# Kernel optimization log

Hardware: AMD Instinct MI355X
Metric: run time of the kernel (lower is better)

Reference implementation:

```python
import jax, jax.numpy as jnp
import numpy as np

H = 512   # LSTM hidden
D = 256   # attention / key dim
V = 33    # output vocab

def _lstm_step(xcat, h, c, W, U, b):
    # Keras LSTMCell: gates ordered i, f, g(candidate), o
    z = xcat @ W + h @ U + b            # [B, 4H]
    i, f, g, o = jnp.split(z, 4, axis=-1)
    i = jax.nn.sigmoid(i); f = jax.nn.sigmoid(f); o = jax.nn.sigmoid(o)
    c_new = f * c + i * jnp.tanh(g)
    h_new = o * jnp.tanh(c_new)
    return h_new, c_new

def _attn(h, keys, Wq, bq):
    # Luong dot attention: query = Dense(h); scores = keys . query; read = softmax . keys
    q = h @ Wq + bq                                # [B, D]
    scores = jnp.einsum('bkd,bd->bk', keys, q)     # [B, K]
    w = jax.nn.softmax(scores, axis=-1)
    return jnp.einsum('bk,bkd->bd', w, keys)       # [B, D]

def setup_inputs() -> dict:
    key = jax.random.key(0)
    ks = jax.random.split(key, 16)
    B, T, K = 256, 256, 512
    s = 0.02
    inp = {
        'x': jax.random.normal(ks[0], (B, T, V), jnp.float32),
        'keys': jax.random.normal(ks[1], (B, K, D), jnp.float32),
        # LSTM 1: input = concat(x[V], attn[D]) -> V+D
        'W1': jax.random.normal(ks[2], (V + D, 4 * H), jnp.float32) * s,
        'U1': jax.random.normal(ks[3], (H, 4 * H), jnp.float32) * s,
        'b1': jnp.zeros((4 * H,), jnp.float32),
        # LSTM 2: input = concat(h1[H], attn1[D]) -> H+D
        'W2': jax.random.normal(ks[4], (H + D, 4 * H), jnp.float32) * s,
        'U2': jax.random.normal(ks[5], (H, 4 * H), jnp.float32) * s,
        'b2': jnp.zeros((4 * H,), jnp.float32),
        # LSTM 3
        'W3': jax.random.normal(ks[6], (H + D, 4 * H), jnp.float32) * s,
        'U3': jax.random.normal(ks[7], (H, 4 * H), jnp.float32) * s,
        'b3': jnp.zeros((4 * H,), jnp.float32),
        # attention query Dense(256) on h[H]
        'Wq': jax.random.normal(ks[8], (H, D), jnp.float32) * s,
        'bq': jnp.zeros((D,), jnp.float32),
        # output Dense(33) on concat(h3[H], attn3[D])
        'Wo': jax.random.normal(ks[9], (H + D, V), jnp.float32) * s,
        'bo': jnp.zeros((V,), jnp.float32),
    }
    return inp

def reference(x, keys, W1, U1, b1, W2, U2, b2, W3, U3, b3, Wq, bq, Wo, bo):
    B, T, _ = x.shape

    def step(carry, x_t):
        h1, c1, h2, c2, h3, c3, a = carry
        inp = jnp.concatenate([x_t, a], axis=-1)          # [B, V+D]
        h1, c1 = _lstm_step(inp, h1, c1, W1, U1, b1)
        a1 = _attn(h1, keys, Wq, bq)
        h2, c2 = _lstm_step(jnp.concatenate([h1, a1], axis=-1), h2, c2, W2, U2, b2)
        a2 = _attn(h2, keys, Wq, bq)
        h3, c3 = _lstm_step(jnp.concatenate([h2, a2], axis=-1), h3, c3, W3, U3, b3)
        a3 = _attn(h3, keys, Wq, bq)
        out = jnp.concatenate([h3, a3], axis=-1) @ Wo + bo  # [B, V]
        return (h1, c1, h2, c2, h3, c3, a3), out

    z = jnp.zeros((B, H), x.dtype)
    carry0 = (z, z, z, z, z, z, jnp.zeros((B, D), x.dtype))
    _, outs = jax.lax.scan(step, carry0, jnp.swapaxes(x, 0, 1))  # outs: [T, B, V]
    return jnp.swapaxes(outs, 0, 1)  # [B, T, V]
```

## Files before the change

kernel.cpp:

```cpp
#include <hip/hip_runtime.h>
#include <hip/hip_bf16.h>
#include <math.h>

#define BB 256
#define TT 256
#define VV 33
#define HH 512
#define DD 256
#define KKEY 512
#define G4 2048
#define K1 832
#define K1A 768
#define K1X 64
#define K2 1280
#define CH 32
#define KP 260

typedef unsigned short u16;
typedef unsigned int u32;
typedef __attribute__((ext_vector_type(8))) short short8;
typedef __attribute__((ext_vector_type(4))) float float4v;

__device__ inline float bf2f(u16 v) {
    union { u32 u; float f; } c; c.u = ((u32)v) << 16; return c.f;
}
__device__ inline u16 f2bf(float f) {
    __hip_bfloat16 h = __float2bfloat16(f);
    union { __hip_bfloat16 h; u16 u; } c; c.h = h; return c.u;
}
__device__ inline void split_bf(float v, u16& hi, u16& lo) {
    hi = f2bf(v);
    lo = f2bf(v - bf2f(hi));
}

__global__ void prep_v7(const float* __restrict__ W, const float* __restrict__ U,
                        u16* __restrict__ WtH, u16* __restrict__ WtL, int Kd, int mode) {
    long idx = (long)blockIdx.x * blockDim.x + threadIdx.x;
    if (idx >= (long)G4 * Kd) return;
    int colp = (int)(idx / Kd);
    int k = (int)(idx % Kd);
    int col = (colp & 3) * 512 + (colp >> 2);
    float v = 0.f;
    if (mode == 1) {
        if (k < 256)      v = W[(long)(33 + k) * G4 + col];
        else if (k < 768) v = U[(long)(k - 256) * G4 + col];
        else if (k < 801) v = W[(long)(k - 768) * G4 + col];
    } else {
        if (k < 768) v = W[(long)k * G4 + col];
        else         v = U[(long)(k - 768) * G4 + col];
    }
    u16 hi, lo; split_bf(v, hi, lo);
    WtH[idx] = hi; WtL[idx] = lo;
}

__global__ void packx_v7(const float* __restrict__ x, u16* __restrict__ xPH, u16* __restrict__ xPL) {
    long idx = (long)blockIdx.x * blockDim.x + threadIdx.x;
    if (idx >= (long)TT * BB * K1X) return;
    int k = (int)(idx % K1X);
    long tb = idx / K1X;
    int b = (int)(tb % BB);
    int t = (int)(tb / BB);
    float v = (k < VV) ? x[((long)b * TT + t) * VV + k] : 0.f;
    u16 hi, lo; split_bf(v, hi, lo);
    xPH[idx] = hi; xPL[idx] = lo;
}

__global__ __launch_bounds__(256, 2) void zg_v8(
    const u16* __restrict__ aH, const u16* __restrict__ aL, int strideA, int Kd,
    const u16* __restrict__ xH, const u16* __restrict__ xL,
    const u16* __restrict__ wH, const u16* __restrict__ wL,
    const float* __restrict__ bias,
    float* __restrict__ c, float* __restrict__ h,
    u16* __restrict__ d0H, u16* __restrict__ d0L, int d0off, int d0stride,
    u16* __restrict__ d1H, u16* __restrict__ d1L, int d1off, int d1stride)
{
    __shared__ u16 AldsH[32 * 40];
    __shared__ u16 AldsL[32 * 40];
    __shared__ u16 WldsH[32 * 40];
    __shared__ u16 WldsL[32 * 40];
    __shared__ float zlds[32 * 36];

    int tid = threadIdx.x;
    int mt = blockIdx.x >> 6;
    int nt = blockIdx.x & 63;
    int M0 = mt * 32, N0 = nt * 32;

    int wave = tid >> 6, lane = tid & 63;
    int lr = lane & 15, lg = lane >> 4;
    int rbase = (wave & 1) * 16, cbase = (wave >> 1) * 16;

    int half = tid >> 7;
    int slot = tid & 127;
    int sr = slot >> 2, sp = slot & 3;

    const u16* aRow = (half ? aL : aH) + (long)(M0 + sr) * strideA;
    const u16* xRow = xH ? ((half ? xL : xH) + (long)(M0 + sr) * K1X) : nullptr;
    const u16* wRow = (half ? wL : wH) + (long)(N0 + sr) * Kd;
    u16* aDst = (half ? AldsL : AldsH) + sr * 40 + sp * 8;
    u16* wDst = (half ? WldsL : WldsH) + sr * 40 + sp * 8;

    float4v acc = (float4v){0.f, 0.f, 0.f, 0.f};

    for (int k0 = 0; k0 < Kd; k0 += 32) {
        int kg = k0 + sp * 8;
        uint4 va = (xRow && kg >= K1A) ? *(const uint4*)(xRow + (kg - K1A))
                                       : *(const uint4*)(aRow + kg);
        uint4 vw = *(const uint4*)(wRow + kg);
        __syncthreads();
        *(uint4*)aDst = va;
        *(uint4*)wDst = vw;
        __syncthreads();
        short8 ah = *(const short8*)(&AldsH[(rbase + lr) * 40 + lg * 8]);
        short8 al = *(const short8*)(&AldsL[(rbase + lr) * 40 + lg * 8]);
        short8 bh = *(const short8*)(&WldsH[(cbase + lr) * 40 + lg * 8]);
        short8 bl = *(const short8*)(&WldsL[(cbase + lr) * 40 + lg * 8]);
        acc = __builtin_amdgcn_mfma_f32_16x16x32_bf16(ah, bh, acc, 0, 0, 0);
        acc = __builtin_amdgcn_mfma_f32_16x16x32_bf16(ah, bl, acc, 0, 0, 0);
        acc = __builtin_amdgcn_mfma_f32_16x16x32_bf16(al, bh, acc, 0, 0, 0);
    }

    #pragma unroll
    for (int r = 0; r < 4; r++)
        zlds[(rbase + lg * 4 + r) * 36 + cbase + lr] = acc[r];
    __syncthreads();

    int um = tid & 7, ml = tid >> 3;
    int u = (nt << 3) + um;
    int m = M0 + ml;
    float zi  = zlds[ml * 36 + um * 4 + 0] + bias[u];
    float zf  = zlds[ml * 36 + um * 4 + 1] + bias[512 + u];
    float zg_ = zlds[ml * 36 + um * 4 + 2] + bias[1024 + u];
    float zo  = zlds[ml * 36 + um * 4 + 3] + bias[1536 + u];
    float i_ = 1.f / (1.f + expf(-zi));
    float f_ = 1.f / (1.f + expf(-zf));
    float g_ = tanhf(zg_);
    float o_ = 1.f / (1.f + expf(-zo));
    long idx = (long)m * HH + u;
    float cn = f_ * c[idx] + i_ * g_;
    c[idx] = cn;
    float hn = o_ * tanhf(cn);
    h[idx] = hn;
    u16 hi_, lo_; split_bf(hn, hi_, lo_);
    if (d0H) {
        d0H[(long)m * d0stride + d0off + u] = hi_;
        d0L[(long)m * d0stride + d0off + u] = lo_;
    }
    d1H[(long)m * d1stride + d1off + u] = hi_;
    d1L[(long)m * d1stride + d1off + u] = lo_;
}

__global__ __launch_bounds__(256) void qattn_v8(
    const float* __restrict__ h, const float* __restrict__ Wq,
    const float* __restrict__ bq, const float* __restrict__ keys,
    u16* __restrict__ dH, u16* __restrict__ dL, int doff, int dstride,
    const float* __restrict__ Wo, const float* __restrict__ bo,
    float* __restrict__ out, int t)
{
    __shared__ __align__(16) float hlds[HH];
    __shared__ __align__(16) float qlds[DD];
    __shared__ __align__(16) float klds[CH * KP];
    __shared__ __align__(16) float slds[CH];
    __shared__ __align__(16) float plds[CH];
    __shared__ __align__(16) float alds[DD];

    int b = blockIdx.x, tid = threadIdx.x;
    int lane = tid & 63, wave = tid >> 6;

    hlds[tid]       = h[(long)b * HH + tid];
    hlds[tid + 256] = h[(long)b * HH + 256 + tid];
    __syncthreads();

    {
        float s0 = 0.f, s1 = 0.f, s2 = 0.f, s3 = 0.f;
        #pragma unroll 8
        for (int j = 0; j < HH; j += 4) {
            s0 += hlds[j]     * Wq[(long)j * DD + tid];
            s1 += hlds[j + 1] * Wq[(long)(j + 1) * DD + tid];
            s2 += hlds[j + 2] * Wq[(long)(j + 2) * DD + tid];
            s3 += hlds[j + 3] * Wq[(long)(j + 3) * DD + tid];
        }
        qlds[tid] = (s0 + s1) + (s2 + s3) + bq[tid];
    }
    __syncthreads();

    const float* kb = keys + (long)b * KKEY * DD;
    float4 q4 = *(const float4*)(&qlds[lane * 4]);

    float m_run = -INFINITY, l_run = 0.f, acc = 0.f;

    float4 kv[8];
    #pragma unroll
    for (int i = 0; i < 8; i++)
        kv[i] = *(const float4*)(kb + (long)(wave + 4 * i) * DD + lane * 4);

    for (int k0 = 0; k0 < KKEY; k0 += CH) {
        __syncthreads();
        float pp[8];
        #pragma unroll
        for (int i = 0; i < 8; i++) {
            *(float4*)(&klds[(wave + 4 * i) * KP + lane * 4]) = kv[i];
            pp[i] = kv[i].x * q4.x + kv[i].y * q4.y + kv[i].z * q4.z + kv[i].w * q4.w;
        }
        float4 kn[8];
        if (k0 + CH < KKEY) {
            #pragma unroll
            for (int i = 0; i < 8; i++)
                kn[i] = *(const float4*)(kb + (long)(k0 + CH + wave + 4 * i) * DD + lane * 4);
        }
        #pragma unroll
        for (int i = 0; i < 8; i++) {
            float s = pp[i];
            s += __shfl_xor(s, 32); s += __shfl_xor(s, 16); s += __shfl_xor(s, 8);
            s += __shfl_xor(s, 4);  s += __shfl_xor(s, 2);  s += __shfl_xor(s, 1);
            if (lane == i) slds[wave + 4 * i] = s;
        }
        __syncthreads();
        float mc = slds[0];
        #pragma unroll
        for (int k = 1; k < CH; k++) mc = fmaxf(mc, slds[k]);
        float m_new = fmaxf(m_run, mc);
        float scale = expf(m_run - m_new);
        if (tid < CH) plds[tid] = expf(slds[tid] - m_new);
        __syncthreads();
        float lsum = 0.f, a0 = 0.f, a1 = 0.f;
        #pragma unroll
        for (int k = 0; k < CH; k += 4) {
            float4 p4 = *(const float4*)(&plds[k]);
            lsum += (p4.x + p4.y) + (p4.z + p4.w);
            a0 += p4.x * klds[(k + 0) * KP + tid] + p4.z * klds[(k + 2) * KP + tid];
            a1 += p4.y * klds[(k + 1) * KP + tid] + p4.w * klds[(k + 3) * KP + tid];
        }
        acc = acc * scale + (a0 + a1);
        l_run = l_run * scale + lsum;
        m_run = m_new;
        #pragma unroll
        for (int i = 0; i < 8; i++) kv[i] = kn[i];
    }

    float av = acc / l_run;
    u16 hi_, lo_; split_bf(av, hi_, lo_);
    dH[(long)b * dstride + doff + tid] = hi_;
    dL[(long)b * dstride + doff + tid] = lo_;

    if (Wo) {
        alds[tid] = av;
        __syncthreads();
        for (int v = wave; v < VV; v += 4) {
            float s = 0.f;
            for (int i = lane; i < HH; i += 64) s += hlds[i] * Wo[(long)i * VV + v];
            for (int i = lane; i < DD; i += 64) s += alds[i] * Wo[(long)(HH + i) * VV + v];
            for (int o = 32; o > 0; o >>= 1) s += __shfl_xor(s, o);
            if (lane == 0) out[((long)b * TT + t) * VV + v] = s + bo[v];
        }
    }
}


extern "C" void kernel_launch(void* const* d_in, const int* in_sizes, int n_in,
                              void* d_out, int out_size, void* d_ws, size_t ws_size,
                              hipStream_t stream) {
    const float *x = nullptr, *keys = nullptr, *W1 = nullptr, *U1 = nullptr,
                *b1 = nullptr, *W2 = nullptr, *U2 = nullptr, *b2 = nullptr,
                *W3 = nullptr, *U3 = nullptr, *b3 = nullptr, *Wq = nullptr,
                *bq = nullptr, *Wo = nullptr, *bo = nullptr;
    {
        int cW23 = 0, cU = 0, cb = 0;
        for (int i = 0; i < n_in; i++) {
            const float* q = (const float*)d_in[i];
            switch (in_sizes[i]) {
                case 2162688:  x = q; break;
                case 33554432: keys = q; break;
                case 591872:   W1 = q; break;
                case 1572864:  if (cW23 == 0) W2 = q; else W3 = q; cW23++; break;
                case 1048576:  if (cU == 0) U1 = q; else if (cU == 1) U2 = q; else U3 = q; cU++; break;
                case 2048:     if (cb == 0) b1 = q; else if (cb == 1) b2 = q; else b3 = q; cb++; break;
                case 131072:   Wq = q; break;
                case 256:      bq = q; break;
                case 25344:    Wo = q; break;
                case 33:       bo = q; break;
                default: break;
            }
        }
    }
    float* out = (float*)d_out;

    char* p = (char*)d_ws;
    auto alloc = [&](size_t n) { char* r = p; p += (n + 255) & ~(size_t)255; return r; };
    u16* WtH1 = (u16*)alloc((size_t)G4 * K1 * 2);
    u16* WtL1 = (u16*)alloc((size_t)G4 * K1 * 2);
    u16* WtH2 = (u16*)alloc((size_t)G4 * K2 * 2);
    u16* WtL2 = (u16*)alloc((size_t)G4 * K2 * 2);
    u16* WtH3 = (u16*)alloc((size_t)G4 * K2 * 2);
    u16* WtL3 = (u16*)alloc((size_t)G4 * K2 * 2);
    u16* xPH = (u16*)alloc((size_t)TT * BB * K1X * 2);
    u16* xPL = (u16*)alloc((size_t)TT * BB * K1X * 2);
    u16* xc1H[2]; u16* xc1L[2]; u16* xc2H[2]; u16* xc2L[2]; u16* xc3H[2]; u16* xc3L[2];
    for (int i = 0; i < 2; i++) {
        xc1H[i] = (u16*)alloc((size_t)BB * K1A * 2);
        xc1L[i] = (u16*)alloc((size_t)BB * K1A * 2);
        xc2H[i] = (u16*)alloc((size_t)BB * K2 * 2);
        xc2L[i] = (u16*)alloc((size_t)BB * K2 * 2);
        xc3H[i] = (u16*)alloc((size_t)BB * K2 * 2);
        xc3L[i] = (u16*)alloc((size_t)BB * K2 * 2);
    }
    float* h1 = (float*)alloc((size_t)BB * HH * 4);
    float* c1 = (float*)alloc((size_t)BB * HH * 4);
    float* h2 = (float*)alloc((size_t)BB * HH * 4);
    float* c2 = (float*)alloc((size_t)BB * HH * 4);
    float* h3 = (float*)alloc((size_t)BB * HH * 4);
    float* c3 = (float*)alloc((size_t)BB * HH * 4);

    {
        long t1 = (long)G4 * K1;
        prep_v7<<<(int)((t1 + 255) / 256), 256, 0, stream>>>(W1, U1, WtH1, WtL1, K1, 1);
        long t2 = (long)G4 * K2;
        prep_v7<<<(int)((t2 + 255) / 256), 256, 0, stream>>>(W2, U2, WtH2, WtL2, K2, 2);
        prep_v7<<<(int)((t2 + 255) / 256), 256, 0, stream>>>(W3, U3, WtH3, WtL3, K2, 2);
        long tx = (long)TT * BB * K1X;
        packx_v7<<<(int)((tx + 255) / 256), 256, 0, stream>>>(x, xPH, xPL);
        hipMemsetAsync(c1, 0, (size_t)BB * HH * 4, stream);
        hipMemsetAsync(c2, 0, (size_t)BB * HH * 4, stream);
        hipMemsetAsync(c3, 0, (size_t)BB * HH * 4, stream);
        hipMemsetAsync(xc1H[0], 0, (size_t)BB * K1A * 2, stream);
        hipMemsetAsync(xc1L[0], 0, (size_t)BB * K1A * 2, stream);
        hipMemsetAsync(xc2H[0], 0, (size_t)BB * K2 * 2, stream);
        hipMemsetAsync(xc2L[0], 0, (size_t)BB * K2 * 2, stream);
        hipMemsetAsync(xc3H[0], 0, (size_t)BB * K2 * 2, stream);
        hipMemsetAsync(xc3L[0], 0, (size_t)BB * K2 * 2, stream);
    }

    for (int t = 0; t < TT; t++) {
        int cur = t & 1, nxt = cur ^ 1;
        zg_v8<<<512, 256, 0, stream>>>(
            xc1H[cur], xc1L[cur], K1A, K1,
            xPH + (long)t * BB * K1X, xPL + (long)t * BB * K1X,
            WtH1, WtL1, b1, c1, h1,
            xc2H[cur], xc2L[cur], 0, K2,
            xc1H[nxt], xc1L[nxt], 256, K1A);
        qattn_v8<<<BB, 256, 0, stream>>>(h1, Wq, bq, keys,
            xc2H[cur], xc2L[cur], 512, K2,
            nullptr, nullptr, nullptr, 0);
        zg_v8<<<512, 256, 0, stream>>>(
            xc2H[cur], xc2L[cur], K2, K2, nullptr, nullptr,
            WtH2, WtL2, b2, c2, h2,
            xc3H[cur], xc3L[cur], 0, K2,
            xc2H[nxt], xc2L[nxt], 768, K2);
        qattn_v8<<<BB, 256, 0, stream>>>(h2, Wq, bq, keys,
            xc3H[cur], xc3L[cur], 512, K2,
            nullptr, nullptr, nullptr, 0);
        zg_v8<<<512, 256, 0, stream>>>(
            xc3H[cur], xc3L[cur], K2, K2, nullptr, nullptr,
            WtH3, WtL3, b3, c3, h3,
            nullptr, nullptr, 0, 0,
            xc3H[nxt], xc3L[nxt], 768, K2);
        qattn_v8<<<BB, 256, 0, stream>>>(h3, Wq, bq, keys,
            xc1H[nxt], xc1L[nxt], 0, K1A,
            Wo, bo, out, t);
    }
}
```

Baseline: 61.20 ms.

## Move attention query projection to MFMA GEMM, prefetch zg tiles, drop softmax max

```diff
diff --git a/kernel.cpp b/kernel.cpp
--- a/kernel.cpp
+++ b/kernel.cpp
@@ -53,6 +53,15 @@
     WtH[idx] = hi; WtL[idx] = lo;
 }
 
+__global__ void prep_wq(const float* __restrict__ Wq,
+                        u16* __restrict__ WqTH, u16* __restrict__ WqTL) {
+    int idx = blockIdx.x * blockDim.x + threadIdx.x;
+    if (idx >= DD * HH) return;
+    int d = idx / HH, j = idx % HH;
+    u16 hi, lo; split_bf(Wq[(long)j * DD + d], hi, lo);
+    WqTH[idx] = hi; WqTL[idx] = lo;
+}
+
 __global__ void packx_v7(const float* __restrict__ x, u16* __restrict__ xPH, u16* __restrict__ xPL) {
     long idx = (long)blockIdx.x * blockDim.x + threadIdx.x;
     if (idx >= (long)TT * BB * K1X) return;
@@ -65,7 +74,7 @@
     xPH[idx] = hi; xPL[idx] = lo;
 }
 
-__global__ __launch_bounds__(256, 2) void zg_v8(
+__global__ __launch_bounds__(256, 2) void zg_v9(
     const u16* __restrict__ aH, const u16* __restrict__ aL, int strideA, int Kd,
     const u16* __restrict__ xH, const u16* __restrict__ xL,
     const u16* __restrict__ wH, const u16* __restrict__ wL,
@@ -99,16 +108,25 @@
     u16* aDst = (half ? AldsL : AldsH) + sr * 40 + sp * 8;
     u16* wDst = (half ? WldsL : WldsH) + sr * 40 + sp * 8;
 
+    auto loadA = [&](int kg) -> uint4 {
+        return (xRow && kg >= K1A) ? *(const uint4*)(xRow + (kg - K1A))
+                                   : *(const uint4*)(aRow + kg);
+    };
+
     float4v acc = (float4v){0.f, 0.f, 0.f, 0.f};
 
+    uint4 va = loadA(sp * 8);
+    uint4 vw = *(const uint4*)(wRow + sp * 8);
+
     for (int k0 = 0; k0 < Kd; k0 += 32) {
-        int kg = k0 + sp * 8;
-        uint4 va = (xRow && kg >= K1A) ? *(const uint4*)(xRow + (kg - K1A))
-                                       : *(const uint4*)(aRow + kg);
-        uint4 vw = *(const uint4*)(wRow + kg);
         __syncthreads();
         *(uint4*)aDst = va;
         *(uint4*)wDst = vw;
+        if (k0 + 32 < Kd) {
+            int kg = k0 + 32 + sp * 8;
+            va = loadA(kg);
+            vw = *(const uint4*)(wRow + kg);
+        }
         __syncthreads();
         short8 ah = *(const short8*)(&AldsH[(rbase + lr) * 40 + lg * 8]);
         short8 al = *(const short8*)(&AldsL[(rbase + lr) * 40 + lg * 8]);
@@ -149,44 +167,85 @@
     d1L[(long)m * d1stride + d1off + u] = lo_;
 }
 
-__global__ __launch_bounds__(256) void qattn_v8(
-    const float* __restrict__ h, const float* __restrict__ Wq,
-    const float* __restrict__ bq, const float* __restrict__ keys,
+__global__ __launch_bounds__(256) void qg_v9(
+    const u16* __restrict__ aH, const u16* __restrict__ aL, int strideA,
+    const u16* __restrict__ wH, const u16* __restrict__ wL,
+    const float* __restrict__ bq, float* __restrict__ qout)
+{
+    __shared__ u16 AldsH[32 * 40];
+    __shared__ u16 AldsL[32 * 40];
+    __shared__ u16 WldsH[32 * 40];
+    __shared__ u16 WldsL[32 * 40];
+
+    int tid = threadIdx.x;
+    int mt = blockIdx.x >> 3;
+    int nt = blockIdx.x & 7;
+    int M0 = mt * 32, N0 = nt * 32;
+
+    int wave = tid >> 6, lane = tid & 63;
+    int lr = lane & 15, lg = lane >> 4;
+    int rbase = (wave & 1) * 16, cbase = (wave >> 1) * 16;
+
+    int half = tid >> 7;
+    int slot = tid & 127;
+    int sr = slot >> 2, sp = slot & 3;
+
+    const u16* aRow = (half ? aL : aH) + (long)(M0 + sr) * strideA;
+    const u16* wRow = (half ? wL : wH) + (long)(N0 + sr) * HH;
+    u16* aDst = (half ? AldsL : AldsH) + sr * 40 + sp * 8;
+    u16* wDst = (half ? WldsL : WldsH) + sr * 40 + sp * 8;
+
+    float4v acc = (float4v){0.f, 0.f, 0.f, 0.f};
+
+    uint4 va = *(const uint4*)(aRow + sp * 8);
+    uint4 vw = *(const uint4*)(wRow + sp * 8);
+
+    for (int k0 = 0; k0 < HH; k0 += 32) {
+        __syncthreads();
+        *(uint4*)aDst = va;
+        *(uint4*)wDst = vw;
+        if (k0 + 32 < HH) {
+            int kg = k0 + 32 + sp * 8;
+            va = *(const uint4*)(aRow + kg);
+            vw = *(const uint4*)(wRow + kg);
+        }
+        __syncthreads();
+        short8 ah = *(const short8*)(&AldsH[(rbase + lr) * 40 + lg * 8]);
+        short8 al = *(const short8*)(&AldsL[(rbase + lr) * 40 + lg * 8]);
+        short8 bh = *(const short8*)(&WldsH[(cbase + lr) * 40 + lg * 8]);
+        short8 bl = *(const short8*)(&WldsL[(cbase + lr) * 40 + lg * 8]);
+        acc = __builtin_amdgcn_mfma_f32_16x16x32_bf16(ah, bh, acc, 0, 0, 0);
+        acc = __builtin_amdgcn_mfma_f32_16x16x32_bf16(ah, bl, acc, 0, 0, 0);
+        acc = __builtin_amdgcn_mfma_f32_16x16x32_bf16(al, bh, acc, 0, 0, 0);
+    }
+
+    #pragma unroll
+    for (int r = 0; r < 4; r++) {
+        int m = M0 + rbase + lg * 4 + r;
+        int col = N0 + cbase + lr;
+        qout[(long)m * DD + col] = acc[r] + bq[col];
+    }
+}
+
+__global__ __launch_bounds__(256) void attn_v9(
+    const float* __restrict__ qv, const float* __restrict__ keys,
     u16* __restrict__ dH, u16* __restrict__ dL, int doff, int dstride,
+    const float* __restrict__ h,
     const float* __restrict__ Wo, const float* __restrict__ bo,
     float* __restrict__ out, int t)
 {
+    __shared__ __align__(16) float klds[CH * KP];
+    __shared__ __align__(16) float plds[CH];
     __shared__ __align__(16) float hlds[HH];
-    __shared__ __align__(16) float qlds[DD];
-    __shared__ __align__(16) float klds[CH * KP];
-    __shared__ __align__(16) float slds[CH];
-    __shared__ __align__(16) float plds[CH];
     __shared__ __align__(16) float alds[DD];
 
     int b = blockIdx.x, tid = threadIdx.x;
     int lane = tid & 63, wave = tid >> 6;
 
-    hlds[tid]       = h[(long)b * HH + tid];
-    hlds[tid + 256] = h[(long)b * HH + 256 + tid];
-    __syncthreads();
-
-    {
-        float s0 = 0.f, s1 = 0.f, s2 = 0.f, s3 = 0.f;
-        #pragma unroll 8
-        for (int j = 0; j < HH; j += 4) {
-            s0 += hlds[j]     * Wq[(long)j * DD + tid];
-            s1 += hlds[j + 1] * Wq[(long)(j + 1) * DD + tid];
-            s2 += hlds[j + 2] * Wq[(long)(j + 2) * DD + tid];
-            s3 += hlds[j + 3] * Wq[(long)(j + 3) * DD + tid];
-        }
-        qlds[tid] = (s0 + s1) + (s2 + s3) + bq[tid];
-    }
-    __syncthreads();
-
     const float* kb = keys + (long)b * KKEY * DD;
-    float4 q4 = *(const float4*)(&qlds[lane * 4]);
-
-    float m_run = -INFINITY, l_run = 0.f, acc = 0.f;
+    float4 q4 = *(const float4*)(qv + (long)b * DD + lane * 4);
+
+    float l_run = 0.f, acc = 0.f;
 
     float4 kv[8];
     #pragma unroll
@@ -212,27 +271,18 @@
             float s = pp[i];
             s += __shfl_xor(s, 32); s += __shfl_xor(s, 16); s += __shfl_xor(s, 8);
             s += __shfl_xor(s, 4);  s += __shfl_xor(s, 2);  s += __shfl_xor(s, 1);
-            if (lane == i) slds[wave + 4 * i] = s;
-        }
-        __syncthreads();
-        float mc = slds[0];
-        #pragma unroll
-        for (int k = 1; k < CH; k++) mc = fmaxf(mc, slds[k]);
-        float m_new = fmaxf(m_run, mc);
-        float scale = expf(m_run - m_new);
-        if (tid < CH) plds[tid] = expf(slds[tid] - m_new);
-        __syncthreads();
-        float lsum = 0.f, a0 = 0.f, a1 = 0.f;
+            if (lane == i) plds[wave + 4 * i] = expf(s);
+        }
+        __syncthreads();
+        float a0 = 0.f, a1 = 0.f;
         #pragma unroll
         for (int k = 0; k < CH; k += 4) {
             float4 p4 = *(const float4*)(&plds[k]);
-            lsum += (p4.x + p4.y) + (p4.z + p4.w);
+            l_run += (p4.x + p4.y) + (p4.z + p4.w);
             a0 += p4.x * klds[(k + 0) * KP + tid] + p4.z * klds[(k + 2) * KP + tid];
             a1 += p4.y * klds[(k + 1) * KP + tid] + p4.w * klds[(k + 3) * KP + tid];
         }
-        acc = acc * scale + (a0 + a1);
-        l_run = l_run * scale + lsum;
-        m_run = m_new;
+        acc += a0 + a1;
         #pragma unroll
         for (int i = 0; i < 8; i++) kv[i] = kn[i];
     }
@@ -244,6 +294,8 @@
 
     if (Wo) {
         alds[tid] = av;
+        hlds[tid]       = h[(long)b * HH + tid];
+        hlds[tid + 256] = h[(long)b * HH + 256 + tid];
         __syncthreads();
         for (int v = wave; v < VV; v += 4) {
             float s = 0.f;
@@ -292,6 +344,8 @@
     u16* WtL2 = (u16*)alloc((size_t)G4 * K2 * 2);
     u16* WtH3 = (u16*)alloc((size_t)G4 * K2 * 2);
     u16* WtL3 = (u16*)alloc((size_t)G4 * K2 * 2);
+    u16* WqTH = (u16*)alloc((size_t)DD * HH * 2);
+    u16* WqTL = (u16*)alloc((size_t)DD * HH * 2);
     u16* xPH = (u16*)alloc((size_t)TT * BB * K1X * 2);
     u16* xPL = (u16*)alloc((size_t)TT * BB * K1X * 2);
     u16* xc1H[2]; u16* xc1L[2]; u16* xc2H[2]; u16* xc2L[2]; u16* xc3H[2]; u16* xc3L[2];
@@ -309,6 +363,7 @@
     float* c2 = (float*)alloc((size_t)BB * HH * 4);
     float* h3 = (float*)alloc((size_t)BB * HH * 4);
     float* c3 = (float*)alloc((size_t)BB * HH * 4);
+    float* qv = (float*)alloc((size_t)BB * DD * 4);
 
     {
         long t1 = (long)G4 * K1;
@@ -316,6 +371,7 @@
         long t2 = (long)G4 * K2;
         prep_v7<<<(int)((t2 + 255) / 256), 256, 0, stream>>>(W2, U2, WtH2, WtL2, K2, 2);
         prep_v7<<<(int)((t2 + 255) / 256), 256, 0, stream>>>(W3, U3, WtH3, WtL3, K2, 2);
+        prep_wq<<<(DD * HH + 255) / 256, 256, 0, stream>>>(Wq, WqTH, WqTL);
         long tx = (long)TT * BB * K1X;
         packx_v7<<<(int)((tx + 255) / 256), 256, 0, stream>>>(x, xPH, xPL);
         hipMemsetAsync(c1, 0, (size_t)BB * HH * 4, stream);
@@ -331,30 +387,36 @@
 
     for (int t = 0; t < TT; t++) {
         int cur = t & 1, nxt = cur ^ 1;
-        zg_v8<<<512, 256, 0, stream>>>(
+        zg_v9<<<512, 256, 0, stream>>>(
             xc1H[cur], xc1L[cur], K1A, K1,
             xPH + (long)t * BB * K1X, xPL + (long)t * BB * K1X,
             WtH1, WtL1, b1, c1, h1,
             xc2H[cur], xc2L[cur], 0, K2,
             xc1H[nxt], xc1L[nxt], 256, K1A);
-        qattn_v8<<<BB, 256, 0, stream>>>(h1, Wq, bq, keys,
+        qg_v9<<<64, 256, 0, stream>>>(
+            xc2H[cur], xc2L[cur], K2, WqTH, WqTL, bq, qv);
+        attn_v9<<<BB, 256, 0, stream>>>(qv, keys,
             xc2H[cur], xc2L[cur], 512, K2,
-            nullptr, nullptr, nullptr, 0);
-        zg_v8<<<512, 256, 0, stream>>>(
+            h1, nullptr, nullptr, nullptr, 0);
+        zg_v9<<<512, 256, 0, stream>>>(
             xc2H[cur], xc2L[cur], K2, K2, nullptr, nullptr,
             WtH2, WtL2, b2, c2, h2,
             xc3H[cur], xc3L[cur], 0, K2,
             xc2H[nxt], xc2L[nxt], 768, K2);
-        qattn_v8<<<BB, 256, 0, stream>>>(h2, Wq, bq, keys,
+        qg_v9<<<64, 256, 0, stream>>>(
+            xc3H[cur], xc3L[cur], K2, WqTH, WqTL, bq, qv);
+        attn_v9<<<BB, 256, 0, stream>>>(qv, keys,
             xc3H[cur], xc3L[cur], 512, K2,
-            nullptr, nullptr, nullptr, 0);
-        zg_v8<<<512, 256, 0, stream>>>(
+            h2, nullptr, nullptr, nullptr, 0);
+        zg_v9<<<512, 256, 0, stream>>>(
             xc3H[cur], xc3L[cur], K2, K2, nullptr, nullptr,
             WtH3, WtL3, b3, c3, h3,
             nullptr, nullptr, 0, 0,
             xc3H[nxt], xc3L[nxt], 768, K2);
-        qattn_v8<<<BB, 256, 0, stream>>>(h3, Wq, bq, keys,
+        qg_v9<<<64, 256, 0, stream>>>(
+            xc3H[nxt] + 768, xc3L[nxt] + 768, K2, WqTH, WqTL, bq, qv);
+        attn_v9<<<BB, 256, 0, stream>>>(qv, keys,
             xc1H[nxt], xc1L[nxt], 0, K1A,
-            Wo, bo, out, t);
-    }
-}
+            h3, Wo, bo, out, t);
+    }
+}
```

After: 60.73 ms. Within noise of the previous version (-0.8%).
